# Performance work log

Measured on AMD Instinct MI355X. Metric: run time of the kernel, lower is better.

The kernel has to match this reference:

```python
import jax, jax.numpy as jnp
import numpy as np

NUM_HEADS = 16
DIM = 1024

def setup_inputs() -> dict:
    key = jax.random.key(0)
    ks = jax.random.split(key, 12)
    B, N, T, C = 4, 4096, 77, DIM
    s = 1.0 / np.sqrt(C)
    return {
        "hidden_states": jax.random.normal(ks[0], (B, N, C), jnp.float32),
        "encoder_hidden_states": jax.random.normal(ks[1], (B, T, C), jnp.float32),
        "attention_mask": jnp.zeros((B, N, T), jnp.float32),
        "Wq": jax.random.normal(ks[2], (C, C), jnp.float32) * s,
        "bq": jnp.zeros((C,), jnp.float32),
        "Wk": jax.random.normal(ks[3], (C, C), jnp.float32) * s,
        "bk": jnp.zeros((C,), jnp.float32),
        "Wv": jax.random.normal(ks[4], (C, C), jnp.float32) * s,
        "bv": jnp.zeros((C,), jnp.float32),
        "Wo": jax.random.normal(ks[5], (C, C), jnp.float32) * s,
        "bo": jnp.zeros((C,), jnp.float32),
    }

def reference(hidden_states, encoder_hidden_states, attention_mask,
              Wq, bq, Wk, bk, Wv, bv, Wo, bo):
    B, N, C = hidden_states.shape
    T = encoder_hidden_states.shape[1]
    H = NUM_HEADS
    D = C // H
    # QKV projections (torch Linear: x @ W.T + b)
    q = (hidden_states @ Wq.T + bq).reshape(B, N, H, D).transpose(0, 2, 1, 3)   # bhnd
    k = (encoder_hidden_states @ Wk.T + bk).reshape(B, T, H, D).transpose(0, 2, 1, 3)  # bhtd
    v = (encoder_hidden_states @ Wv.T + bv).reshape(B, T, H, D).transpose(0, 2, 1, 3)  # bhtd
    scale = 1.0 / jnp.sqrt(jnp.asarray(D, q.dtype))
    # scores [B,H,N,T]; additive mask broadcast over heads
    scores = jnp.einsum('bhnd,bhtd->bhnt', q, k) * scale + attention_mask[:, None, :, :]
    attn = jax.nn.softmax(scores, axis=-1)
    out = jnp.einsum('bhnt,bhtd->bhnd', attn, v)
    out = out.transpose(0, 2, 1, 3).reshape(B, N, C)
    return out @ Wo.T + bo
```

## Files before the change

### kernel.cpp

```cpp
#include <hip/hip_runtime.h>
#include <cstdint>

typedef __bf16 bf16x8 __attribute__((ext_vector_type(8)));
typedef float f32x4 __attribute__((ext_vector_type(4)));
typedef unsigned short u16;
typedef unsigned int u32;

__device__ __forceinline__ u16 f2bf(float f) {
    u32 u = __builtin_bit_cast(u32, f);
    u += 0x7fffu + ((u >> 16) & 1u);
    return (u16)(u >> 16);
}

__device__ __forceinline__ void gl_lds16(const u16* g, u16* l) {
    __builtin_amdgcn_global_load_lds(
        (const __attribute__((address_space(1))) void*)g,
        (__attribute__((address_space(3))) void*)l,
        16, 0, 0);
}

__device__ __forceinline__ f32x4 mfma16(bf16x8 a, bf16x8 b, f32x4 c) {
    return __builtin_amdgcn_mfma_f32_16x16x32_bf16(a, b, c, 0, 0, 0);
}

__global__ void cvt_pad(const float* __restrict__ src, u16* __restrict__ dst,
                        int srcn, int totn) {
    int i = (blockIdx.x * 256 + threadIdx.x) * 4;
    if (i >= totn) return;
    float4 v = make_float4(0.f, 0.f, 0.f, 0.f);
    if (i < srcn) v = *(const float4*)&src[i];
    ushort4 o;
    o.x = f2bf(v.x); o.y = f2bf(v.y); o.z = f2bf(v.z); o.w = f2bf(v.w);
    *(ushort4*)&dst[i] = o;
}

struct CvtArgs {
    const float* s[5];
    u16* d[5];
    int srcn[5];
    int totn[5];
};

__global__ void cvt_multi(CvtArgs a) {
    const int seg = blockIdx.y;
    int i = (blockIdx.x * 256 + threadIdx.x) * 4;
    if (i >= a.totn[seg]) return;
    float4 v = make_float4(0.f, 0.f, 0.f, 0.f);
    if (i < a.srcn[seg]) v = *(const float4*)&a.s[seg][i];
    ushort4 o;
    o.x = f2bf(v.x); o.y = f2bf(v.y); o.z = f2bf(v.z); o.w = f2bf(v.w);
    *(ushort4*)&a.d[seg][i] = o;
}

__device__ __forceinline__ void store_out(u16* C, long idx, float v) { C[idx] = f2bf(v); }
__device__ __forceinline__ void store_out(float* C, long idx, float v) { C[idx] = v; }

template <typename OutT>
__global__ __launch_bounds__(512, 2) void gemm256(
    const u16* __restrict__ A, const u16* __restrict__ W,
    const float* __restrict__ bias, OutT* __restrict__ C,
    int M, int N, int K) {
    __shared__ __align__(16) u16 As[3][256 * 64];
    __shared__ __align__(16) u16 Bs[3][128 * 64];

    const int tid = threadIdx.x;
    const int wid = tid >> 6, l = tid & 63;
    const int wr = wid >> 1, wc = wid & 1;
    const int l15 = l & 15, lg = l >> 4;

    const int nwg = gridDim.x * gridDim.y;
    const int lin = blockIdx.y * gridDim.x + blockIdx.x;
    const int cpx = nwg >> 3;
    const int swz = (lin & 7) * cpx + (lin >> 3);
    const long tn = swz % gridDim.x;
    const long tm = swz / gridDim.x;

    const u16* Ab = A + tm * 256 * (long)K;
    const u16* Bb = W + tn * 128 * (long)K;

    const int srow = tid >> 3;
    const int schunk = tid & 7;
    const int swch = schunk ^ (srow & 7);
    const long asrc = (long)srow * K + swch * 8;

    const int NT = K >> 6;

#define STAGE(bufi, k0)                                                        \
    do {                                                                       \
        u16* ab_ = &As[bufi][0];                                               \
        u16* bb_ = &Bs[bufi][0];                                               \
        _Pragma("unroll")                                                      \
        for (int j_ = 0; j_ < 4; ++j_)                                         \
            gl_lds16(Ab + (long)(j_ * 64) * K + asrc + (k0),                   \
                     ab_ + j_ * 4096 + tid * 8);                               \
        _Pragma("unroll")                                                      \
        for (int j_ = 0; j_ < 2; ++j_)                                         \
            gl_lds16(Bb + (long)(j_ * 64) * K + asrc + (k0),                   \
                     bb_ + j_ * 4096 + tid * 8);                               \
    } while (0)

    f32x4 acc[4][4] = {};

    STAGE(0, 0);
    STAGE(1, 64);

    const int rchunk = lg;
    const int rsw = l15 & 7;

    for (int t = 0; t < NT; ++t) {
        if (t + 1 < NT) {
            asm volatile("s_waitcnt vmcnt(6)" ::: "memory");
        } else {
            asm volatile("s_waitcnt vmcnt(0)" ::: "memory");
        }
        __builtin_amdgcn_sched_barrier(0);
        __builtin_amdgcn_s_barrier();

        const int buf = t % 3;
        if (t + 2 < NT) {
            const int nb = (t + 2) % 3;
            STAGE(nb, (t + 2) << 6);
        }

        bf16x8 a[4][2], b[4][2];
#pragma unroll
        for (int m = 0; m < 4; ++m) {
            const int row = wr * 64 + m * 16 + l15;
#pragma unroll
            for (int kk = 0; kk < 2; ++kk) {
                const int c = (kk * 4 + rchunk) ^ rsw;
                a[m][kk] = *(const bf16x8*)&As[buf][row * 64 + c * 8];
            }
        }
#pragma unroll
        for (int n = 0; n < 4; ++n) {
            const int row = wc * 64 + n * 16 + l15;
#pragma unroll
            for (int kk = 0; kk < 2; ++kk) {
                const int c = (kk * 4 + rchunk) ^ rsw;
                b[n][kk] = *(const bf16x8*)&Bs[buf][row * 64 + c * 8];
            }
        }

        __builtin_amdgcn_s_setprio(1);
#pragma unroll
        for (int m = 0; m < 4; ++m)
#pragma unroll
            for (int n = 0; n < 4; ++n) {
                acc[m][n] = mfma16(a[m][0], b[n][0], acc[m][n]);
                acc[m][n] = mfma16(a[m][1], b[n][1], acc[m][n]);
            }
        __builtin_amdgcn_s_setprio(0);
    }
#undef STAGE

    const long row0 = tm * 256 + wr * 64;
    const long col0 = tn * 128 + wc * 64;
#pragma unroll
    for (int m = 0; m < 4; ++m)
#pragma unroll
        for (int n = 0; n < 4; ++n)
#pragma unroll
            for (int r = 0; r < 4; ++r) {
                const long row = row0 + m * 16 + lg * 4 + r;
                const long col = col0 + n * 16 + l15;
                store_out(C, row * N + col, acc[m][n][r] + bias[col]);
            }
}

__device__ __forceinline__ void gemm128_body(
    const u16* __restrict__ A, const u16* __restrict__ W,
    const float* __restrict__ bias, u16* __restrict__ C,
    int N, int K) {
    __shared__ u16 As[128 * 64];
    __shared__ u16 Bs[128 * 64];
    const int tid = threadIdx.x;
    const int w = tid >> 6, l = tid & 63;
    const int wr = w >> 1, wc = w & 1;
    const int l15 = l & 15, lg = l >> 4;
    const long tm = blockIdx.y, tn = blockIdx.x;
    const u16* Ab = A + tm * 128 * (long)K;
    const u16* Bb = W + tn * 128 * (long)K;

    f32x4 acc[4][4] = {};

    for (int k0 = 0; k0 < K; k0 += 64) {
#pragma unroll
        for (int t = 0; t < 4; ++t) {
            int i = t * 256 + tid;
            int row = i >> 3, cc = i & 7;
            gl_lds16(Ab + (long)row * K + k0 + cc * 8, &As[i * 8]);
            gl_lds16(Bb + (long)row * K + k0 + cc * 8, &Bs[i * 8]);
        }
        __syncthreads();
#pragma unroll
        for (int kk = 0; kk < 64; kk += 32) {
            bf16x8 a[4], b[4];
#pragma unroll
            for (int m = 0; m < 4; ++m)
                a[m] = *(const bf16x8*)&As[(wr * 64 + m * 16 + l15) * 64 + kk + lg * 8];
#pragma unroll
            for (int n = 0; n < 4; ++n)
                b[n] = *(const bf16x8*)&Bs[(wc * 64 + n * 16 + l15) * 64 + kk + lg * 8];
#pragma unroll
            for (int m = 0; m < 4; ++m)
#pragma unroll
                for (int n = 0; n < 4; ++n)
                    acc[m][n] = mfma16(a[m], b[n], acc[m][n]);
        }
        __syncthreads();
    }

    const long row0 = tm * 128 + wr * 64;
    const long col0 = tn * 128 + wc * 64;
#pragma unroll
    for (int m = 0; m < 4; ++m)
#pragma unroll
        for (int n = 0; n < 4; ++n)
#pragma unroll
            for (int r = 0; r < 4; ++r) {
                const long row = row0 + m * 16 + lg * 4 + r;
                const long col = col0 + n * 16 + l15;
                C[row * N + col] = f2bf(acc[m][n][r] + bias[col]);
            }
}

__global__ __launch_bounds__(256) void gemm_kv(
    const u16* __restrict__ A,
    const u16* __restrict__ Wk, const float* __restrict__ bk, u16* __restrict__ Ko,
    const u16* __restrict__ Wv, const float* __restrict__ bv, u16* __restrict__ Vo,
    int N, int K) {
    const bool isv = blockIdx.z != 0;
    gemm128_body(A, isv ? Wv : Wk, isv ? bv : bk, isv ? Vo : Ko, N, K);
}

__global__ __launch_bounds__(256) void attn_fused(
    const u16* __restrict__ Q,
    const u16* __restrict__ Kb,
    const u16* __restrict__ Vb,
    const float* __restrict__ mask,
    u16* __restrict__ Ao) {
    __shared__ u16 Ks[96 * 64];
    __shared__ u16 Vt[64 * 96];
    __shared__ u16 Ps[128 * 96];

    const int b = blockIdx.z, h = blockIdx.y, nt = blockIdx.x;
    const int tid = threadIdx.x;
    const int w = tid >> 6, l = tid & 63;
    const int l15 = l & 15, lg = l >> 4;

    for (int c = tid; c < 768; c += 256) {
        const int t = c >> 3, dc = c & 7;
        union { uint4 u; u16 s[8]; } kv, vv;
        kv.u = make_uint4(0, 0, 0, 0);
        vv.u = make_uint4(0, 0, 0, 0);
        if (t < 77) {
            const long base = ((long)(b * 77 + t)) * 1024 + h * 64 + dc * 8;
            kv.u = *(const uint4*)&Kb[base];
            vv.u = *(const uint4*)&Vb[base];
        }
        *(uint4*)&Ks[t * 64 + dc * 8] = kv.u;
#pragma unroll
        for (int j = 0; j < 8; ++j) Vt[(dc * 8 + j) * 96 + t] = vv.s[j];
    }
    __syncthreads();

    f32x4 acc[2][6] = {};
    const long qrow0 = (long)b * 4096 + nt * 128 + w * 32;
#pragma unroll
    for (int kk = 0; kk < 64; kk += 32) {
        bf16x8 a[2], kf[6];
#pragma unroll
        for (int m = 0; m < 2; ++m)
            a[m] = *(const bf16x8*)&Q[(qrow0 + m * 16 + l15) * 1024 + h * 64 + kk + lg * 8];
#pragma unroll
        for (int n = 0; n < 6; ++n)
            kf[n] = *(const bf16x8*)&Ks[(n * 16 + l15) * 64 + kk + lg * 8];
#pragma unroll
        for (int m = 0; m < 2; ++m)
#pragma unroll
            for (int n = 0; n < 6; ++n)
                acc[m][n] = mfma16(a[m], kf[n], acc[m][n]);
    }

    const float* mbase = mask + ((long)b * 4096 + nt * 128 + w * 32) * 77;
#pragma unroll
    for (int m = 0; m < 2; ++m) {
#pragma unroll
        for (int r = 0; r < 4; ++r) {
            const int row = m * 16 + lg * 4 + r;
            float vals[6];
            float rmax = -3e38f;
#pragma unroll
            for (int n = 0; n < 6; ++n) {
                const int col = n * 16 + l15;
                float v = -3e38f;
                if (col < 77) v = acc[m][n][r] * 0.125f + mbase[row * 77 + col];
                vals[n] = v;
                rmax = fmaxf(rmax, v);
            }
#pragma unroll
            for (int off = 1; off < 16; off <<= 1)
                rmax = fmaxf(rmax, __shfl_xor(rmax, off, 64));
            float s = 0.f;
#pragma unroll
            for (int n = 0; n < 6; ++n) {
                float e = (vals[n] > -1e37f) ? __expf(vals[n] - rmax) : 0.f;
                vals[n] = e;
                s += e;
            }
#pragma unroll
            for (int off = 1; off < 16; off <<= 1)
                s += __shfl_xor(s, off, 64);
            const float inv = 1.f / s;
#pragma unroll
            for (int n = 0; n < 6; ++n)
                Ps[(w * 32 + row) * 96 + n * 16 + l15] = f2bf(vals[n] * inv);
        }
    }
    __syncthreads();

    f32x4 o[2][4] = {};
#pragma unroll
    for (int kt = 0; kt < 96; kt += 32) {
        bf16x8 a[2], vf[4];
#pragma unroll
        for (int m = 0; m < 2; ++m)
            a[m] = *(const bf16x8*)&Ps[(w * 32 + m * 16 + l15) * 96 + kt + lg * 8];
#pragma unroll
        for (int n = 0; n < 4; ++n)
            vf[n] = *(const bf16x8*)&Vt[(n * 16 + l15) * 96 + kt + lg * 8];
#pragma unroll
        for (int m = 0; m < 2; ++m)
#pragma unroll
            for (int n = 0; n < 4; ++n)
                o[m][n] = mfma16(a[m], vf[n], o[m][n]);
    }

#pragma unroll
    for (int m = 0; m < 2; ++m)
#pragma unroll
        for (int n = 0; n < 4; ++n)
#pragma unroll
            for (int r = 0; r < 4; ++r) {
                const long row = (long)b * 4096 + nt * 128 + w * 32 + m * 16 + lg * 4 + r;
                const int col = h * 64 + n * 16 + l15;
                Ao[row * 1024 + col] = f2bf(o[m][n][r]);
            }
}

extern "C" void kernel_launch(void* const* d_in, const int* in_sizes, int n_in,
                              void* d_out, int out_size, void* d_ws, size_t ws_size,
                              hipStream_t stream) {
    const float* hidden = (const float*)d_in[0];
    const float* enc = (const float*)d_in[1];
    const float* mask = (const float*)d_in[2];
    const float* Wq = (const float*)d_in[3];
    const float* bq = (const float*)d_in[4];
    const float* Wk = (const float*)d_in[5];
    const float* bk = (const float*)d_in[6];
    const float* Wv = (const float*)d_in[7];
    const float* bv = (const float*)d_in[8];
    const float* Wo = (const float*)d_in[9];
    const float* bo = (const float*)d_in[10];
    float* out = (float*)d_out;

    char* ws = (char*)d_ws;
    u16* hiddenB = (u16*)(ws);
    u16* Qb = (u16*)(ws + 33554432L);
    u16* AoB = (u16*)(ws + 2 * 33554432L);
    u16* WqB = (u16*)(ws + 3 * 33554432L);
    u16* WkB = WqB + 1048576;
    u16* WvB = WkB + 1048576;
    u16* WoB = WvB + 1048576;
    u16* encB = WoB + 1048576;
    u16* Kbuf = encB + 393216;
    u16* Vbuf = Kbuf + 393216;

    cvt_pad<<<dim3(16384), 256, 0, stream>>>(hidden, hiddenB, 16777216, 16777216);
    CvtArgs ca;
    ca.s[0] = Wq;  ca.d[0] = WqB; ca.srcn[0] = 1048576; ca.totn[0] = 1048576;
    ca.s[1] = Wk;  ca.d[1] = WkB; ca.srcn[1] = 1048576; ca.totn[1] = 1048576;
    ca.s[2] = Wv;  ca.d[2] = WvB; ca.srcn[2] = 1048576; ca.totn[2] = 1048576;
    ca.s[3] = Wo;  ca.d[3] = WoB; ca.srcn[3] = 1048576; ca.totn[3] = 1048576;
    ca.s[4] = enc; ca.d[4] = encB; ca.srcn[4] = 315392; ca.totn[4] = 393216;
    cvt_multi<<<dim3(1024, 5), 256, 0, stream>>>(ca);

    gemm256<u16><<<dim3(8, 64), 512, 0, stream>>>(hiddenB, WqB, bq, Qb, 16384, 1024, 1024);
    gemm_kv<<<dim3(8, 3, 2), 256, 0, stream>>>(encB, WkB, bk, Kbuf, WvB, bv, Vbuf, 1024, 1024);

    attn_fused<<<dim3(32, 16, 4), 256, 0, stream>>>(Qb, Kbuf, Vbuf, mask, AoB);

    gemm256<float><<<dim3(8, 64), 512, 0, stream>>>(AoB, WoB, bo, out, 16384, 1024, 1024);
}
```

Before: 187.5 us.

## Restructure projection GEMM to 256x256 tiles with split-phase 8-wave pipeline

Replaces the 256x128 tile, 3-stage K=64 GEMM with a 256x256 tile using K=32 steps and a 4-slot LDS ring. Each wave computes 128x64 in two MFMA phases, and the A and B prefetch loads are interleaved between those phases with extra barriers, in the style of an 8-wave ping-pong schedule. This halves the grid to 256 blocks and raises operand reuse per loaded byte, at the cost of more accumulator registers, more barriers, and fewer blocks to fill the CUs. The bias values are also hoisted into registers before the store loop.

```diff
diff --git a/kernel.cpp b/kernel.cpp
--- a/kernel.cpp
+++ b/kernel.cpp
@@ -56,115 +56,124 @@
 __device__ __forceinline__ void store_out(float* C, long idx, float v) { C[idx] = v; }
 
 template <typename OutT>
-__global__ __launch_bounds__(512, 2) void gemm256(
+__global__ __launch_bounds__(512, 2) void gemm8p(
     const u16* __restrict__ A, const u16* __restrict__ W,
     const float* __restrict__ bias, OutT* __restrict__ C,
     int M, int N, int K) {
-    __shared__ __align__(16) u16 As[3][256 * 64];
-    __shared__ __align__(16) u16 Bs[3][128 * 64];
+    __shared__ __align__(16) u16 As[4][256 * 32];
+    __shared__ __align__(16) u16 Bs[4][256 * 32];
 
     const int tid = threadIdx.x;
     const int wid = tid >> 6, l = tid & 63;
-    const int wr = wid >> 1, wc = wid & 1;
+    const int wr = wid >> 2, wc = wid & 3;
     const int l15 = l & 15, lg = l >> 4;
 
-    const int nwg = gridDim.x * gridDim.y;
     const int lin = blockIdx.y * gridDim.x + blockIdx.x;
-    const int cpx = nwg >> 3;
+    const int cpx = (gridDim.x * gridDim.y) >> 3;
     const int swz = (lin & 7) * cpx + (lin >> 3);
     const long tn = swz % gridDim.x;
     const long tm = swz / gridDim.x;
 
     const u16* Ab = A + tm * 256 * (long)K;
-    const u16* Bb = W + tn * 128 * (long)K;
-
-    const int srow = tid >> 3;
-    const int schunk = tid & 7;
-    const int swch = schunk ^ (srow & 7);
-    const long asrc = (long)srow * K + swch * 8;
-
-    const int NT = K >> 6;
-
-#define STAGE(bufi, k0)                                                        \
-    do {                                                                       \
-        u16* ab_ = &As[bufi][0];                                               \
-        u16* bb_ = &Bs[bufi][0];                                               \
-        _Pragma("unroll")                                                      \
-        for (int j_ = 0; j_ < 4; ++j_)                                         \
-            gl_lds16(Ab + (long)(j_ * 64) * K + asrc + (k0),                   \
-                     ab_ + j_ * 4096 + tid * 8);                               \
-        _Pragma("unroll")                                                      \
-        for (int j_ = 0; j_ < 2; ++j_)                                         \
-            gl_lds16(Bb + (long)(j_ * 64) * K + asrc + (k0),                   \
-                     bb_ + j_ * 4096 + tid * 8);                               \
+    const u16* Bb = W + tn * 256 * (long)K;
+
+    const int srow = tid >> 2;
+    const int sch = (tid & 3) ^ (srow & 3) ^ ((srow >> 2) & 3);
+    const long asrc = (long)srow * K + sch * 8;
+
+    const int rch = (lg ^ (l15 & 3) ^ ((l15 >> 2) & 3)) * 8;
+
+    const int NT = K >> 5;
+
+#define STAGE_A(ss, t_)                                                       \
+    do {                                                                      \
+        u16* p_ = &As[ss][0];                                                 \
+        gl_lds16(Ab + asrc + (long)(t_)*32, p_ + tid * 8);                    \
+        gl_lds16(Ab + 128L * K + asrc + (long)(t_)*32, p_ + 4096 + tid * 8);  \
     } while (0)
-
-    f32x4 acc[4][4] = {};
-
-    STAGE(0, 0);
-    STAGE(1, 64);
-
-    const int rchunk = lg;
-    const int rsw = l15 & 7;
-
-    for (int t = 0; t < NT; ++t) {
-        if (t + 1 < NT) {
-            asm volatile("s_waitcnt vmcnt(6)" ::: "memory");
-        } else {
-            asm volatile("s_waitcnt vmcnt(0)" ::: "memory");
+#define STAGE_B(ss, t_)                                                       \
+    do {                                                                      \
+        u16* p_ = &Bs[ss][0];                                                 \
+        gl_lds16(Bb + asrc + (long)(t_)*32, p_ + tid * 8);                    \
+        gl_lds16(Bb + 128L * K + asrc + (long)(t_)*32, p_ + 4096 + tid * 8);  \
+    } while (0)
+
+    f32x4 acc[8][4] = {};
+
+    STAGE_A(0, 0); STAGE_B(0, 0);
+    STAGE_A(1, 1); STAGE_B(1, 1);
+    asm volatile("s_waitcnt vmcnt(4)" ::: "memory");
+    __builtin_amdgcn_sched_barrier(0);
+    __builtin_amdgcn_s_barrier();
+
+    for (int t0 = 0; t0 < NT; t0 += 4) {
+#pragma unroll
+        for (int u = 0; u < 4; ++u) {
+            const int t = t0 + u;
+            const int slot = u;
+            const int ss = (u + 2) & 3;
+            const bool st = (t + 2) < NT;
+
+            bf16x8 a[4], b[4];
+#pragma unroll
+            for (int mf = 0; mf < 4; ++mf)
+                a[mf] = *(const bf16x8*)&As[slot][(wr * 128 + mf * 16 + l15) * 32 + rch];
+#pragma unroll
+            for (int nf = 0; nf < 4; ++nf)
+                b[nf] = *(const bf16x8*)&Bs[slot][(wc * 64 + nf * 16 + l15) * 32 + rch];
+            if (st) STAGE_A(ss, t + 2);
+            __builtin_amdgcn_s_barrier();
+            asm volatile("s_waitcnt lgkmcnt(0)" ::: "memory");
+            __builtin_amdgcn_sched_barrier(0);
+            __builtin_amdgcn_s_setprio(1);
+#pragma unroll
+            for (int mf = 0; mf < 4; ++mf)
+#pragma unroll
+                for (int nf = 0; nf < 4; ++nf)
+                    acc[mf][nf] = mfma16(a[mf], b[nf], acc[mf][nf]);
+            __builtin_amdgcn_s_setprio(0);
+            __builtin_amdgcn_s_barrier();
+
+            bf16x8 a2[4];
+#pragma unroll
+            for (int mf = 0; mf < 4; ++mf)
+                a2[mf] = *(const bf16x8*)&As[slot][(wr * 128 + (mf + 4) * 16 + l15) * 32 + rch];
+            if (st) STAGE_B(ss, t + 2);
+            __builtin_amdgcn_s_barrier();
+            asm volatile("s_waitcnt lgkmcnt(0)" ::: "memory");
+            __builtin_amdgcn_sched_barrier(0);
+            __builtin_amdgcn_s_setprio(1);
+#pragma unroll
+            for (int mf = 0; mf < 4; ++mf)
+#pragma unroll
+                for (int nf = 0; nf < 4; ++nf)
+                    acc[mf + 4][nf] = mfma16(a2[mf], b[nf], acc[mf + 4][nf]);
+            __builtin_amdgcn_s_setprio(0);
+            if (st)
+                asm volatile("s_waitcnt vmcnt(4)" ::: "memory");
+            else
+                asm volatile("s_waitcnt vmcnt(0)" ::: "memory");
+            __builtin_amdgcn_sched_barrier(0);
+            __builtin_amdgcn_s_barrier();
         }
-        __builtin_amdgcn_sched_barrier(0);
-        __builtin_amdgcn_s_barrier();
-
-        const int buf = t % 3;
-        if (t + 2 < NT) {
-            const int nb = (t + 2) % 3;
-            STAGE(nb, (t + 2) << 6);
-        }
-
-        bf16x8 a[4][2], b[4][2];
-#pragma unroll
-        for (int m = 0; m < 4; ++m) {
-            const int row = wr * 64 + m * 16 + l15;
-#pragma unroll
-            for (int kk = 0; kk < 2; ++kk) {
-                const int c = (kk * 4 + rchunk) ^ rsw;
-                a[m][kk] = *(const bf16x8*)&As[buf][row * 64 + c * 8];
-            }
-        }
-#pragma unroll
-        for (int n = 0; n < 4; ++n) {
-            const int row = wc * 64 + n * 16 + l15;
-#pragma unroll
-            for (int kk = 0; kk < 2; ++kk) {
-                const int c = (kk * 4 + rchunk) ^ rsw;
-                b[n][kk] = *(const bf16x8*)&Bs[buf][row * 64 + c * 8];
-            }
-        }
-
-        __builtin_amdgcn_s_setprio(1);
-#pragma unroll
-        for (int m = 0; m < 4; ++m)
-#pragma unroll
-            for (int n = 0; n < 4; ++n) {
-                acc[m][n] = mfma16(a[m][0], b[n][0], acc[m][n]);
-                acc[m][n] = mfma16(a[m][1], b[n][1], acc[m][n]);
-            }
-        __builtin_amdgcn_s_setprio(0);
-    }
-#undef STAGE
-
-    const long row0 = tm * 256 + wr * 64;
-    const long col0 = tn * 128 + wc * 64;
-#pragma unroll
-    for (int m = 0; m < 4; ++m)
-#pragma unroll
-        for (int n = 0; n < 4; ++n)
+    }
+#undef STAGE_A
+#undef STAGE_B
+
+    const long row0 = tm * 256 + wr * 128;
+    const long col0 = tn * 256 + wc * 64;
+    float bv[4];
+#pragma unroll
+    for (int nf = 0; nf < 4; ++nf) bv[nf] = bias[col0 + nf * 16 + l15];
+#pragma unroll
+    for (int mf = 0; mf < 8; ++mf)
+#pragma unroll
+        for (int nf = 0; nf < 4; ++nf)
 #pragma unroll
             for (int r = 0; r < 4; ++r) {
-                const long row = row0 + m * 16 + lg * 4 + r;
-                const long col = col0 + n * 16 + l15;
-                store_out(C, row * N + col, acc[m][n][r] + bias[col]);
+                const long row = row0 + mf * 16 + lg * 4 + r;
+                const long col = col0 + nf * 16 + l15;
+                store_out(C, row * N + col, acc[mf][nf][r] + bv[nf]);
             }
 }
 
@@ -386,10 +395,10 @@
     ca.s[4] = enc; ca.d[4] = encB; ca.srcn[4] = 315392; ca.totn[4] = 393216;
     cvt_multi<<<dim3(1024, 5), 256, 0, stream>>>(ca);
 
-    gemm256<u16><<<dim3(8, 64), 512, 0, stream>>>(hiddenB, WqB, bq, Qb, 16384, 1024, 1024);
+    gemm8p<u16><<<dim3(4, 64), 512, 0, stream>>>(hiddenB, WqB, bq, Qb, 16384, 1024, 1024);
     gemm_kv<<<dim3(8, 3, 2), 256, 0, stream>>>(encB, WkB, bk, Kbuf, WvB, bv, Vbuf, 1024, 1024);
 
     attn_fused<<<dim3(32, 16, 4), 256, 0, stream>>>(Qb, Kbuf, Vbuf, mask, AoB);
 
-    gemm256<float><<<dim3(8, 64), 512, 0, stream>>>(AoB, WoB, bo, out, 16384, 1024, 1024);
-}
+    gemm8p<float><<<dim3(4, 64), 512, 0, stream>>>(AoB, WoB, bo, out, 16384, 1024, 1024);
+}
```

After: 171.8 us. -8.3%, faster.
